# Kernel optimization log

Hardware: AMD Instinct MI355X
Metric: run time of the kernel (lower is better)

Reference implementation:

```python
import jax, jax.numpy as jnp
import numpy as np

IN_SHAPE = 8192
OUT_SHAPE = 32
BATCH = 16384


def setup_inputs() -> dict:
    key = jax.random.key(0)
    kx, kw = jax.random.split(key)
    x = jax.random.normal(kx, (BATCH, IN_SHAPE), dtype=jnp.float32)
    # matches torch init: (rand*2-1)*0.001 -> uniform(-0.001, 0.001)
    weight = jax.random.uniform(kw, (OUT_SHAPE, IN_SHAPE), dtype=jnp.float32,
                                minval=-0.001, maxval=0.001)
    return {"x": x, "weight": weight}


def _binarize(weight):
    # scale = mean(|W|), detached
    scale = jax.lax.stop_gradient(jnp.mean(jnp.abs(weight)))
    clipped = jnp.clip(weight, -1.0, 1.0)
    # STE: forward value = scale*sign(W); gradient flows through clipped W
    return jax.lax.stop_gradient(scale * jnp.sign(weight) - clipped) + clipped


def reference(x, weight):
    bw = _binarize(weight)            # [out, in]
    return x @ bw.T                   # [batch, out]
```

## Files before the change

kernel.cpp:

```cpp
#include <hip/hip_runtime.h>

#define BATCH 16384
#define KDIM  8192
#define ODIM  32
#define SK    8
#define KSLICE (KDIM / SK)
#define KT    32
#define NTILE (KSLICE / KT)
#define THREADS 256

typedef short bf16x8 __attribute__((ext_vector_type(8)));
typedef float f32x16 __attribute__((ext_vector_type(16)));

__device__ __forceinline__ void gload16(const float* g, void* l) {
    __builtin_amdgcn_global_load_lds(
        (const __attribute__((address_space(1))) void*)g,
        (__attribute__((address_space(3))) void*)l, 16, 0, 0);
}

__global__ void prep_kernel(const float* __restrict__ w,
                            unsigned short* __restrict__ bwTo,
                            float* __restrict__ partial) {
    int idx = blockIdx.x * 256 + threadIdx.x;
    float v = w[idx];
    bwTo[idx] = (v > 0.f) ? 0x3F80u : ((v < 0.f) ? 0xBF80u : 0u);

    float a = fabsf(v);
    #pragma unroll
    for (int off = 32; off; off >>= 1) a += __shfl_down(a, off, 64);
    __shared__ float red[4];
    int lane = threadIdx.x & 63, wv = threadIdx.x >> 6;
    if (lane == 0) red[wv] = a;
    __syncthreads();
    if (threadIdx.x == 0)
        partial[blockIdx.x] = (red[0] + red[1]) + (red[2] + red[3]);
}

__global__ __launch_bounds__(THREADS, 8)
void main_kernel(const float* __restrict__ x,
                 const unsigned short* __restrict__ bwTo,
                 float* __restrict__ pout) {
    __shared__ union {
        float buf[2][64][KT];
        float part[2][64][33];
    } sm;

    const int tid  = threadIdx.x;
    const int wv   = __builtin_amdgcn_readfirstlane(tid >> 6);
    const int lane = tid & 63;
    const int l31  = lane & 31, lhi = lane >> 5;
    const int kH   = wv & 1;
    const int rH   = wv >> 1;
    const int kb   = blockIdx.x & 7;
    const int rb   = blockIdx.x >> 3;
    const size_t rowbase = (size_t)rb * 64;
    const int kbase = kb * KSLICE;

    const int srow   = lane >> 3;
    const int schunk = (lane & 7) ^ srow;
    const float* __restrict__ g0 =
        x + (rowbase + 16 * wv + srow) * (size_t)KDIM + kbase + 4 * schunk;
    const float* __restrict__ g1 = g0 + (size_t)8 * KDIM;
    void* const d0a = &sm.buf[0][16 * wv][0];
    void* const d0b = &sm.buf[0][16 * wv + 8][0];
    void* const d1a = &sm.buf[1][16 * wv][0];
    void* const d1b = &sm.buf[1][16 * wv + 8][0];

    const unsigned short* __restrict__ bp =
        bwTo + (size_t)l31 * KDIM + kbase + kH * 16 + lhi * 8;

    const int arow  = rH * 32 + l31;
    const int slot0 = ((kH << 2) | (lhi << 1)) ^ (arow & 7);
    const int slot1 = slot0 ^ 1;

    f32x16 acc;
    #pragma unroll
    for (int i = 0; i < 16; ++i) acc[i] = 0.f;

#define ISSUE(db, t) do {                                        \
        if (db) { gload16(g0 + (t) * KT, d1a);                   \
                  gload16(g1 + (t) * KT, d1b); }                 \
        else    { gload16(g0 + (t) * KT, d0a);                   \
                  gload16(g1 + (t) * KT, d0b); }                 \
    } while (0)

    ISSUE(0, 0);
    bf16x8 bcur = *(const bf16x8*)bp;

    for (int t = 0; t < NTILE; ++t) {
        __syncthreads();

        if (t + 1 < NTILE) ISSUE((t + 1) & 1, t + 1);
        bf16x8 bnext;
        if (t + 1 < NTILE) bnext = *(const bf16x8*)(bp + (t + 1) * KT);

        const float4 xa = *(const float4*)&sm.buf[t & 1][arow][slot0 * 4];
        const float4 xb = *(const float4*)&sm.buf[t & 1][arow][slot1 * 4];
        bf16x8 ahi, alo;
        {
            const float xf[8] = {xa.x, xa.y, xa.z, xa.w, xb.x, xb.y, xb.z, xb.w};
            #pragma unroll
            for (int j = 0; j < 8; ++j) {
                unsigned bu = __float_as_uint(xf[j]);
                float lo = xf[j] - __uint_as_float(bu & 0xFFFF0000u);
                ahi[j] = (short)(bu >> 16);
                alo[j] = (short)(__float_as_uint(lo) >> 16);
            }
        }

        acc = __builtin_amdgcn_mfma_f32_32x32x16_bf16(ahi, bcur, acc, 0, 0, 0);
        acc = __builtin_amdgcn_mfma_f32_32x32x16_bf16(alo, bcur, acc, 0, 0, 0);
        bcur = bnext;
    }
#undef ISSUE

    __syncthreads();
    #pragma unroll
    for (int r = 0; r < 16; ++r) {
        int row32 = (r & 3) + 8 * (r >> 2) + 4 * lhi;
        sm.part[kH][rH * 32 + row32][l31] = acc[r];
    }
    __syncthreads();

    float* __restrict__ pb = pout + ((size_t)kb * BATCH + rowbase) * ODIM;
    #pragma unroll
    for (int i = 0; i < 8; ++i) {
        int j = tid + THREADS * i;
        int r = j >> 5, o = j & 31;
        pb[j] = sm.part[0][r][o] + sm.part[1][r][o];
    }
}

__global__ void reduce_kernel(const float* __restrict__ pout,
                              const float* __restrict__ partial,
                              float* __restrict__ out) {
    const int t = threadIdx.x;
    float a = (partial[t] + partial[t + 256]) + (partial[t + 512] + partial[t + 768]);
    #pragma unroll
    for (int off = 32; off; off >>= 1) a += __shfl_down(a, off, 64);
    __shared__ float red[4];
    __shared__ float sbc;
    if ((t & 63) == 0) red[t >> 6] = a;
    __syncthreads();
    if (t == 0)
        sbc = ((red[0] + red[1]) + (red[2] + red[3])) / (float)(ODIM * KDIM);
    __syncthreads();
    const float s = sbc;

    const int STRIDE = BATCH * ODIM / 4;
    int i = blockIdx.x * 256 + t;
    const float4* p = (const float4*)pout;
    float4 r = p[i];
    #pragma unroll
    for (int k = 1; k < SK; ++k) {
        float4 A = p[i + k * STRIDE];
        r.x += A.x; r.y += A.y; r.z += A.z; r.w += A.w;
    }
    r.x *= s; r.y *= s; r.z *= s; r.w *= s;
    ((float4*)out)[i] = r;
}

extern "C" void kernel_launch(void* const* d_in, const int* in_sizes, int n_in,
                              void* d_out, int out_size, void* d_ws, size_t ws_size,
                              hipStream_t stream) {
    const float* x = (const float*)d_in[0];
    const float* w = (const float*)d_in[1];
    float* out = (float*)d_out;

    float* wsf = (float*)d_ws;
    float* partial       = wsf;
    unsigned short* bwTo = (unsigned short*)(wsf + 1024);
    float* pout          = wsf + 1024 + (ODIM * KDIM / 2);

    prep_kernel<<<1024, 256, 0, stream>>>(w, bwTo, partial);
    main_kernel<<<256 * SK, THREADS, 0, stream>>>(x, bwTo, pout);
    reduce_kernel<<<BATCH * ODIM / 4 / 256, 256, 0, stream>>>(pout, partial, out);
}
```

Before: 142.1 us.

## Give each wave a private K-half and register-staged LDS pipeline without block barriers

Each wave now owns its own 32-row by half-K-slice region. It loads x tiles into registers, writes them to a per-wave double-buffered LDS area, and issues two MFMA pairs per iteration. Global-to-LDS direct loads and the per-tile __syncthreads are dropped, and data is prefetched two tiles ahead in registers. This is meant to remove block-wide synchronisation and deepen the memory pipeline. The cost is more registers (launch bounds lowered to 6) and reliance on wave-local ordering of LDS writes and reads, with no explicit barrier between them.

```diff
diff --git a/kernel.cpp b/kernel.cpp
--- a/kernel.cpp
+++ b/kernel.cpp
@@ -5,18 +5,13 @@
 #define ODIM  32
 #define SK    8
 #define KSLICE (KDIM / SK)
+#define KHALF  (KSLICE / 2)
 #define KT    32
-#define NTILE (KSLICE / KT)
+#define NT    (KHALF / KT)
 #define THREADS 256
 
 typedef short bf16x8 __attribute__((ext_vector_type(8)));
 typedef float f32x16 __attribute__((ext_vector_type(16)));
-
-__device__ __forceinline__ void gload16(const float* g, void* l) {
-    __builtin_amdgcn_global_load_lds(
-        (const __attribute__((address_space(1))) void*)g,
-        (__attribute__((address_space(3))) void*)l, 16, 0, 0);
-}
 
 __global__ void prep_kernel(const float* __restrict__ w,
                             unsigned short* __restrict__ bwTo,
@@ -36,12 +31,12 @@
         partial[blockIdx.x] = (red[0] + red[1]) + (red[2] + red[3]);
 }
 
-__global__ __launch_bounds__(THREADS, 8)
+__global__ __launch_bounds__(THREADS, 6)
 void main_kernel(const float* __restrict__ x,
                  const unsigned short* __restrict__ bwTo,
                  float* __restrict__ pout) {
     __shared__ union {
-        float buf[2][64][KT];
+        float buf[4][2][32][KT];
         float part[2][64][33];
     } sm;
 
@@ -54,65 +49,90 @@
     const int kb   = blockIdx.x & 7;
     const int rb   = blockIdx.x >> 3;
     const size_t rowbase = (size_t)rb * 64;
-    const int kbase = kb * KSLICE;
+    const int kbase = kb * KSLICE + kH * KHALF;
 
-    const int srow   = lane >> 3;
-    const int schunk = (lane & 7) ^ srow;
+    const int srow8 = lane >> 3;
+    const int sc    = lane & 7;
+    const int ssl   = sc ^ srow8;
     const float* __restrict__ g0 =
-        x + (rowbase + 16 * wv + srow) * (size_t)KDIM + kbase + 4 * schunk;
-    const float* __restrict__ g1 = g0 + (size_t)8 * KDIM;
-    void* const d0a = &sm.buf[0][16 * wv][0];
-    void* const d0b = &sm.buf[0][16 * wv + 8][0];
-    void* const d1a = &sm.buf[1][16 * wv][0];
-    void* const d1b = &sm.buf[1][16 * wv + 8][0];
+        x + (rowbase + rH * 32 + srow8) * (size_t)KDIM + kbase + 4 * sc;
+    const float* __restrict__ g1 = g0 + (size_t)8  * KDIM;
+    const float* __restrict__ g2 = g0 + (size_t)16 * KDIM;
+    const float* __restrict__ g3 = g0 + (size_t)24 * KDIM;
 
     const unsigned short* __restrict__ bp =
-        bwTo + (size_t)l31 * KDIM + kbase + kH * 16 + lhi * 8;
+        bwTo + (size_t)l31 * KDIM + kbase + lhi * 8;
 
-    const int arow  = rH * 32 + l31;
-    const int slot0 = ((kH << 2) | (lhi << 1)) ^ (arow & 7);
-    const int slot1 = slot0 ^ 1;
+    const int m7 = l31 & 7;
+    const int ro00 = 4 * ((0 + 2 * lhi) ^ m7);
+    const int ro01 = 4 * ((1 + 2 * lhi) ^ m7);
+    const int ro10 = 4 * ((4 + 2 * lhi) ^ m7);
+    const int ro11 = 4 * ((5 + 2 * lhi) ^ m7);
+    const float* const rb0 = &sm.buf[wv][0][l31][0];
+    const float* const rb1 = &sm.buf[wv][1][l31][0];
 
     f32x16 acc;
     #pragma unroll
     for (int i = 0; i < 16; ++i) acc[i] = 0.f;
 
-#define ISSUE(db, t) do {                                        \
-        if (db) { gload16(g0 + (t) * KT, d1a);                   \
-                  gload16(g1 + (t) * KT, d1b); }                 \
-        else    { gload16(g0 + (t) * KT, d0a);                   \
-                  gload16(g1 + (t) * KT, d0b); }                 \
+    float4 st0, st1, st2, st3;
+#define LOADT(t) do {                               \
+        st0 = *(const float4*)(g0 + (t) * KT);      \
+        st1 = *(const float4*)(g1 + (t) * KT);      \
+        st2 = *(const float4*)(g2 + (t) * KT);      \
+        st3 = *(const float4*)(g3 + (t) * KT);      \
+    } while (0)
+#define WRITET(db) do {                                         \
+        *(float4*)&sm.buf[wv][db][srow8     ][4 * ssl] = st0;   \
+        *(float4*)&sm.buf[wv][db][srow8 +  8][4 * ssl] = st1;   \
+        *(float4*)&sm.buf[wv][db][srow8 + 16][4 * ssl] = st2;   \
+        *(float4*)&sm.buf[wv][db][srow8 + 24][4 * ssl] = st3;   \
     } while (0)
 
-    ISSUE(0, 0);
-    bf16x8 bcur = *(const bf16x8*)bp;
+    bf16x8 ahi, alo;
+#define STEP(base, o0, o1, bfr) do {                                      \
+        const float4 xa = *(const float4*)((base) + (o0));                \
+        const float4 xb = *(const float4*)((base) + (o1));                \
+        const float xf[8] = {xa.x, xa.y, xa.z, xa.w,                      \
+                             xb.x, xb.y, xb.z, xb.w};                     \
+        _Pragma("unroll")                                                 \
+        for (int j = 0; j < 8; ++j) {                                     \
+            unsigned bu = __float_as_uint(xf[j]);                         \
+            float lo = xf[j] - __uint_as_float(bu & 0xFFFF0000u);         \
+            ahi[j] = (short)(bu >> 16);                                   \
+            alo[j] = (short)(__float_as_uint(lo) >> 16);                  \
+        }                                                                 \
+        acc = __builtin_amdgcn_mfma_f32_32x32x16_bf16(ahi, bfr, acc, 0, 0, 0); \
+        acc = __builtin_amdgcn_mfma_f32_32x32x16_bf16(alo, bfr, acc, 0, 0, 0); \
+    } while (0)
 
-    for (int t = 0; t < NTILE; ++t) {
-        __syncthreads();
+    LOADT(0);
+    WRITET(0);
+    LOADT(1);
+    bf16x8 b0 = *(const bf16x8*)(bp);
+    bf16x8 b1 = *(const bf16x8*)(bp + 16);
 
-        if (t + 1 < NTILE) ISSUE((t + 1) & 1, t + 1);
-        bf16x8 bnext;
-        if (t + 1 < NTILE) bnext = *(const bf16x8*)(bp + (t + 1) * KT);
+    for (int t = 0; t < NT; ++t) {
+        const int db = t & 1;
+        const float* base = db ? rb1 : rb0;
 
-        const float4 xa = *(const float4*)&sm.buf[t & 1][arow][slot0 * 4];
-        const float4 xb = *(const float4*)&sm.buf[t & 1][arow][slot1 * 4];
-        bf16x8 ahi, alo;
-        {
-            const float xf[8] = {xa.x, xa.y, xa.z, xa.w, xb.x, xb.y, xb.z, xb.w};
-            #pragma unroll
-            for (int j = 0; j < 8; ++j) {
-                unsigned bu = __float_as_uint(xf[j]);
-                float lo = xf[j] - __uint_as_float(bu & 0xFFFF0000u);
-                ahi[j] = (short)(bu >> 16);
-                alo[j] = (short)(__float_as_uint(lo) >> 16);
-            }
+        STEP(base, ro00, ro01, b0);
+
+        bf16x8 bn0, bn1;
+        if (t + 1 < NT) {
+            bn0 = *(const bf16x8*)(bp + (t + 1) * KT);
+            bn1 = *(const bf16x8*)(bp + (t + 1) * KT + 16);
         }
 
-        acc = __builtin_amdgcn_mfma_f32_32x32x16_bf16(ahi, bcur, acc, 0, 0, 0);
-        acc = __builtin_amdgcn_mfma_f32_32x32x16_bf16(alo, bcur, acc, 0, 0, 0);
-        bcur = bnext;
+        STEP(base, ro10, ro11, b1);
+
+        if (t + 1 < NT) WRITET(db ^ 1);
+        if (t + 2 < NT) LOADT(t + 2);
+        b0 = bn0; b1 = bn1;
     }
-#undef ISSUE
+#undef LOADT
+#undef WRITET
+#undef STEP
 
     __syncthreads();
     #pragma unroll
```

Result: faster. 126.5 us (-10.9%).
